# Kernel optimization log

Measured on AMD Instinct MI355X. Metric: run time of the kernel, lower is better.

The kernel has to match this reference:

```python
import jax, jax.numpy as jnp
import numpy as np

D = 16        # d_model
DFF = 128     # ffn hidden
H_NN = 128    # pairwise-MLP hidden
RES = 1.0     # res_ratio (undefined global in source; standard residual)
EPS = 1e-6


def setup_inputs() -> dict:
    key = jax.random.key(0)
    ks = jax.random.split(key, 16)
    B, G, L = 8, 1, 256
    def n(k, shape, s=0.05):
        return jax.random.normal(k, shape, jnp.float32) * s
    return dict(
        x=jax.random.normal(ks[0], (B, G, L, D), jnp.float32),
        mask=jnp.zeros((B, G, L, L), jnp.float32),
        wq=n(ks[1], (D, D)), bq=jnp.zeros((D,), jnp.float32),
        wk=n(ks[2], (D, D)), bk=jnp.zeros((D,), jnp.float32),
        wv=n(ks[3], (D, D)), bv=jnp.zeros((D,), jnp.float32),
        wo=n(ks[4], (D, D)), bo=jnp.zeros((D,), jnp.float32),
        nn_w1=n(ks[5], (2 * D, H_NN)), nn_b1=jnp.zeros((H_NN,), jnp.float32),
        nn_w2=n(ks[6], (H_NN, 1)), nn_b2=jnp.zeros((1,), jnp.float32),
        f1=n(ks[7], (D, DFF)), f1b=jnp.zeros((DFF,), jnp.float32),
        f2=n(ks[8], (DFF, D)), f2b=jnp.zeros((D,), jnp.float32),
        g1=jnp.ones((D,), jnp.float32), be1=jnp.zeros((D,), jnp.float32),
        g2=jnp.ones((D,), jnp.float32), be2=jnp.zeros((D,), jnp.float32),
    )


def _layernorm(x, g, b):
    m = jnp.mean(x, -1, keepdims=True)
    v = jnp.var(x, -1, keepdims=True)
    return (x - m) * jax.lax.rsqrt(v + EPS) * g + b


def reference(x, mask, wq, bq, wk, bk, wv, bv, wo, bo,
              nn_w1, nn_b1, nn_w2, nn_b2,
              f1, f1b, f2, f2b, g1, be1, g2, be2):
    # projections: (B,G,L,D)
    q = x @ wq + bq
    k = x @ wk + bk
    v = x @ wv + bv
    # pairwise relation-network attention.
    # NN(concat([q_i, k_j])) first layer splits as q_i @ W1[:D] + k_j @ W1[D:]
    w1q, w1k = nn_w1[:D], nn_w1[D:]
    w2 = nn_w2[:, 0]
    qa = q @ w1q  # (B,G,L,H)
    kb = k @ w1k
    h1 = jax.nn.relu(qa[:, :, :, None, :] + kb[:, :, None, :, :] + nn_b1)  # (B,G,Lq,Lk,H)
    logits = jnp.einsum('bgijh,h->bgij', h1, w2) + nn_b2[0]
    # make_sym: NN(concat([k_j, q_i])) -> k_j @ W1[:D] + q_i @ W1[D:]
    ka = k @ w1q
    qb = q @ w1k
    h2 = jax.nn.relu(qb[:, :, :, None, :] + ka[:, :, None, :, :] + nn_b1)
    logits = logits + jnp.einsum('bgijh,h->bgij', h2, w2) + nn_b2[0]
    logits = logits + mask * -1e9
    attn = jax.nn.softmax(logits, axis=-1)          # (B,G,Lq,Lk)
    ctx = jnp.einsum('bgij,bgjd->bgid', attn, v)    # (B,G,L,D)
    attn_out = ctx @ wo + bo
    out1 = _layernorm(RES * x + (2.0 - RES) * attn_out, g1, be1)
    ffn = jax.nn.relu(out1 @ f1 + f1b) @ f2 + f2b
    out2 = _layernorm(RES * out1 + (2.0 - RES) * ffn, g2, be2)
    return out2
```

## Files before the change

kernel.cpp:

```cpp
#include <hip/hip_runtime.h>
#include <hip/hip_bf16.h>

typedef __hip_bfloat16 bf16;
typedef float f32x4 __attribute__((ext_vector_type(4)));

constexpr int DIM  = 16;
constexpr int HNN  = 128;
constexpr int SEQ  = 256;
constexpr int BAT  = 8;
constexpr int ROWS = BAT * SEQ;
constexpr int HP   = HNN / 2;
constexpr int QT   = 4;
constexpr int NQT  = ROWS / QT;

__device__ __forceinline__ bool is_f32(const void* g1) {
  return ((const unsigned*)g1)[0] == 0x3F800000u;
}
__device__ __forceinline__ float ld(const void* p, long i, bool f32) {
  return f32 ? ((const float*)p)[i]
             : __bfloat162float(((const bf16*)p)[i]);
}

__global__ __launch_bounds__(128) void prep_kernel(
    const void* __restrict__ x,
    const void* __restrict__ wq, const void* __restrict__ bq,
    const void* __restrict__ wk, const void* __restrict__ bk,
    const void* __restrict__ wv, const void* __restrict__ bv,
    const void* __restrict__ nn_w1, const void* __restrict__ nn_b1,
    const void* __restrict__ nn_w2, const void* __restrict__ g1flag,
    float* __restrict__ kkT, float* __restrict__ qq,
    float* __restrict__ vT,  float2* __restrict__ w2p)
{
  const bool f32 = is_f32(g1flag);
  const int row = blockIdx.x;
  const int tid = threadIdx.x;
  __shared__ float xs[DIM], qs[DIM], ks[DIM], vs[DIM];

  if (tid < DIM) xs[tid] = ld(x, (long)row * DIM + tid, f32);
  __syncthreads();

  if (tid < 3 * DIM) {
    const int which = tid >> 4, d = tid & 15;
    const void* w  = (which == 0) ? wq : (which == 1) ? wk : wv;
    const void* bb = (which == 0) ? bq : (which == 1) ? bk : bv;
    float acc = ld(bb, d, f32);
    #pragma unroll
    for (int e = 0; e < DIM; e++) acc += xs[e] * ld(w, e * DIM + d, f32);
    if (which == 0) qs[d] = acc;
    else if (which == 1) ks[d] = acc;
    else vs[d] = acc;
  }
  __syncthreads();

  float qw1q = 0.f, qw1k = 0.f, kw1q = 0.f, kw1k = 0.f;
  #pragma unroll
  for (int d = 0; d < DIM; d++) {
    float a = ld(nn_w1, d * HNN + tid, f32);
    float b = ld(nn_w1, (DIM + d) * HNN + tid, f32);
    qw1q += qs[d] * a;  qw1k += qs[d] * b;
    kw1q += ks[d] * a;  kw1k += ks[d] * b;
  }
  const float b1 = ld(nn_b1, tid, f32);
  const int hp = tid >> 1, half = tid & 1;
  ((float2*)kkT)[((size_t)hp * ROWS + row) * 2 + half] =
      make_float2(kw1k + b1, kw1q + b1);
  ((float2*)qq)[((size_t)row * HP + hp) * 2 + half] =
      make_float2(qw1q, qw1k);
  if (tid < DIM) vT[tid * ROWS + row] = vs[tid];
  if (row == 0 && tid < HP)
    w2p[tid] = make_float2(ld(nn_w2, 2 * tid, f32), ld(nn_w2, 2 * tid + 1, f32));
}

__global__ __launch_bounds__(256) void fused_kernel(
    const void* __restrict__ x,  const void* __restrict__ mask,
    const void* __restrict__ wo, const void* __restrict__ bo,
    const void* __restrict__ nn_b2,
    const void* __restrict__ f1, const void* __restrict__ f1b,
    const void* __restrict__ f2, const void* __restrict__ f2b,
    const void* __restrict__ g1, const void* __restrict__ be1,
    const void* __restrict__ g2, const void* __restrict__ be2,
    const f32x4* __restrict__ kkT, const f32x4* __restrict__ qq,
    const float2* __restrict__ w2p, const float* __restrict__ vT,
    void* __restrict__ out)
{
  const bool f32 = is_f32(g1);
  const int qt   = blockIdx.x;
  const int bi   = qt >> 6;
  const int i0   = (qt & 63) * QT;
  const int row0 = bi * SEQ + i0;
  const int j    = threadIdx.x;
  const int col  = bi * SEQ + j;
  const int lane = j & 63, wv = j >> 6;

  __shared__ float pb[QT][SEQ];
  __shared__ float vbuf[SEQ][DIM + 1];
  __shared__ float cpart[QT][DIM][17];
  __shared__ float mxs[QT], sums[QT];
  __shared__ float ctxs[QT][DIM], o1s[QT][DIM], rrs[QT][DIM];
  __shared__ float hid[QT][HNN];

  #pragma unroll
  for (int d = 0; d < DIM; ++d) vbuf[j][d] = vT[d * ROWS + col];

  const f32x4* kkbase = kkT + col;
  const f32x4* q0b = qq + (size_t)(row0 + 0) * HP;
  const f32x4* q1b = qq + (size_t)(row0 + 1) * HP;
  const f32x4* q2b = qq + (size_t)(row0 + 2) * HP;
  const f32x4* q3b = qq + (size_t)(row0 + 3) * HP;

  const f32x4 z = {0.f, 0.f, 0.f, 0.f};
  f32x4 a0 = z, a1 = z, a2 = z, a3 = z;

  #pragma unroll 4
  for (int m = 0; m < HP; ++m) {
    const f32x4 kk = kkbase[(size_t)m * ROWS];
    const float2 w = w2p[m];
    const f32x4 w4 = {w.x, w.x, w.y, w.y};
    const f32x4 q0 = q0b[m];
    const f32x4 q1 = q1b[m];
    const f32x4 q2 = q2b[m];
    const f32x4 q3 = q3b[m];
    a0 = __builtin_elementwise_fma(__builtin_elementwise_max(q0 + kk, z), w4, a0);
    a1 = __builtin_elementwise_fma(__builtin_elementwise_max(q1 + kk, z), w4, a1);
    a2 = __builtin_elementwise_fma(__builtin_elementwise_max(q2 + kk, z), w4, a2);
    a3 = __builtin_elementwise_fma(__builtin_elementwise_max(q3 + kk, z), w4, a3);
  }

  const float b2 = 2.f * ld(nn_b2, 0, f32);
  float l0 = a0.x + a0.y + a0.z + a0.w + b2
           + ld(mask, (size_t)(row0 + 0) * SEQ + j, f32) * -1e9f;
  float l1 = a1.x + a1.y + a1.z + a1.w + b2
           + ld(mask, (size_t)(row0 + 1) * SEQ + j, f32) * -1e9f;
  float l2 = a2.x + a2.y + a2.z + a2.w + b2
           + ld(mask, (size_t)(row0 + 2) * SEQ + j, f32) * -1e9f;
  float l3 = a3.x + a3.y + a3.z + a3.w + b2
           + ld(mask, (size_t)(row0 + 3) * SEQ + j, f32) * -1e9f;

  pb[0][j] = l0; pb[1][j] = l1; pb[2][j] = l2; pb[3][j] = l3;
  __syncthreads();

  {
    float m4 = fmaxf(fmaxf(pb[wv][lane],       pb[wv][lane + 64]),
                     fmaxf(pb[wv][lane + 128], pb[wv][lane + 192]));
    #pragma unroll
    for (int off = 32; off > 0; off >>= 1) m4 = fmaxf(m4, __shfl_xor(m4, off, 64));
    if (lane == 0) mxs[wv] = m4;
  }
  __syncthreads();
  pb[0][j] = __expf(l0 - mxs[0]);
  pb[1][j] = __expf(l1 - mxs[1]);
  pb[2][j] = __expf(l2 - mxs[2]);
  pb[3][j] = __expf(l3 - mxs[3]);
  __syncthreads();
  {
    float s4 = pb[wv][lane] + pb[wv][lane + 64]
             + pb[wv][lane + 128] + pb[wv][lane + 192];
    #pragma unroll
    for (int off = 32; off > 0; off >>= 1) s4 += __shfl_xor(s4, off, 64);
    if (lane == 0) sums[wv] = s4;
  }
  __syncthreads();

  {
    const int d = j & 15, c = j >> 4;
    #pragma unroll
    for (int i = 0; i < QT; ++i) {
      float s = 0.f;
      #pragma unroll
      for (int jj = 0; jj < 16; ++jj)
        s += pb[i][c * 16 + jj] * vbuf[c * 16 + jj][d];
      cpart[i][d][c] = s;
    }
  }
  __syncthreads();
  if (j < QT * DIM) {
    const int i = j >> 4, d = j & 15;
    float s = 0.f;
    #pragma unroll
    for (int c = 0; c < 16; ++c) s += cpart[i][d][c];
    ctxs[i][d] = s / sums[i];
  }
  __syncthreads();

  if (j < QT * DIM) {
    const int i = j >> 4, d = j & 15;
    float ao = ld(bo, d, f32);
    #pragma unroll
    for (int dd = 0; dd < DIM; ++dd) ao += ctxs[i][dd] * ld(wo, dd * DIM + d, f32);
    rrs[i][d] = ld(x, (long)(row0 + i) * DIM + d, f32) + ao;
  }
  __syncthreads();
  if (j < QT * DIM) {
    const int i = j >> 4, d = j & 15;
    float mn = 0.f;
    #pragma unroll
    for (int dd = 0; dd < DIM; ++dd) mn += rrs[i][dd];
    mn *= (1.f / DIM);
    float vv = 0.f;
    #pragma unroll
    for (int dd = 0; dd < DIM; ++dd) { float zz = rrs[i][dd] - mn; vv += zz * zz; }
    vv *= (1.f / DIM);
    o1s[i][d] = (rrs[i][d] - mn) * rsqrtf(vv + 1e-6f) * ld(g1, d, f32)
              + ld(be1, d, f32);
  }
  __syncthreads();

  #pragma unroll
  for (int r = 0; r < 2; ++r) {
    const int u = r * 256 + j;
    const int i = u >> 7, h = u & 127;
    float a = ld(f1b, h, f32);
    #pragma unroll
    for (int dd = 0; dd < DIM; ++dd) a += o1s[i][dd] * ld(f1, dd * HNN + h, f32);
    hid[i][h] = fmaxf(a, 0.f);
  }
  __syncthreads();

  {
    const int d = j & 15, c = j >> 4;
    #pragma unroll
    for (int i = 0; i < QT; ++i) {
      float a = 0.f;
      #pragma unroll
      for (int hh = 0; hh < 8; ++hh) {
        const int h = c * 8 + hh;
        a += hid[i][h] * ld(f2, h * DIM + d, f32);
      }
      cpart[i][d][c] = a;
    }
  }
  __syncthreads();
  if (j < QT * DIM) {
    const int i = j >> 4, d = j & 15;
    float a = ld(f2b, d, f32);
    #pragma unroll
    for (int c = 0; c < 16; ++c) a += cpart[i][d][c];
    rrs[i][d] = o1s[i][d] + a;
  }
  __syncthreads();

  if (j < QT * DIM) {
    const int i = j >> 4, d = j & 15;
    float mn = 0.f;
    #pragma unroll
    for (int dd = 0; dd < DIM; ++dd) mn += rrs[i][dd];
    mn *= (1.f / DIM);
    float vv = 0.f;
    #pragma unroll
    for (int dd = 0; dd < DIM; ++dd) { float zz = rrs[i][dd] - mn; vv += zz * zz; }
    vv *= (1.f / DIM);
    const float val = (rrs[i][d] - mn) * rsqrtf(vv + 1e-6f) * ld(g2, d, f32)
                    + ld(be2, d, f32);
    const long oidx = (long)(row0 + i) * DIM + d;
    if (f32) ((float*)out)[oidx] = val;
    else     ((bf16*)out)[oidx] = __float2bfloat16(val);
  }
}

extern "C" void kernel_launch(void* const* d_in, const int* in_sizes, int n_in,
                              void* d_out, int out_size, void* d_ws, size_t ws_size,
                              hipStream_t stream) {
  const void* x     = d_in[0];
  const void* mask  = d_in[1];
  const void* wq    = d_in[2];
  const void* bq    = d_in[3];
  const void* wk    = d_in[4];
  const void* bk    = d_in[5];
  const void* wv    = d_in[6];
  const void* bv    = d_in[7];
  const void* wo    = d_in[8];
  const void* bo    = d_in[9];
  const void* nn_w1 = d_in[10];
  const void* nn_b1 = d_in[11];
  const void* nn_w2 = d_in[12];
  const void* nn_b2 = d_in[13];
  const void* f1    = d_in[14];
  const void* f1b   = d_in[15];
  const void* f2    = d_in[16];
  const void* f2b   = d_in[17];
  const void* g1    = d_in[18];
  const void* be1   = d_in[19];
  const void* g2    = d_in[20];
  const void* be2   = d_in[21];

  float*  kkT = (float*)d_ws;
  float*  qq  = kkT + (size_t)HP * ROWS * 4;
  float*  vT  = qq  + (size_t)ROWS * HP * 4;
  float2* w2p = (float2*)(vT + (size_t)DIM * ROWS);

  prep_kernel<<<ROWS, 128, 0, stream>>>(x, wq, bq, wk, bk, wv, bv,
                                        nn_w1, nn_b1, nn_w2, g1,
                                        kkT, qq, vT, w2p);
  fused_kernel<<<NQT, 256, 0, stream>>>(x, mask, wo, bo, nn_b2,
                                        f1, f1b, f2, f2b, g1, be1, g2, be2,
                                        (const f32x4*)kkT, (const f32x4*)qq,
                                        (const float2*)w2p, vT, d_out);
}
```

Baseline: 122.3 us.

## Assign one wavefront per query row and replace block barriers with shuffles

After the logits barrier, each of the four wavefronts now handles one query row on its own: softmax, the context reduction, the output projection, both layernorms and the FFN, all using wave shuffles and a per-row shared buffer. This drops about ten __syncthreads and the shared partial-sum arrays, and the partially idle block phases where only 64 threads worked. Block indexing is also interleaved across batches (bi = b&7) to change how blocks map to batch rows. The trade-off is more serial work per lane in the context and FFN loops, plus reliance on wave-level LDS visibility without a barrier.

Result: faster. 118.3 us (-3.2%).

```diff
diff --git a/kernel.cpp b/kernel.cpp
--- a/kernel.cpp
+++ b/kernel.cpp
@@ -84,9 +84,9 @@
     void* __restrict__ out)
 {
   const bool f32 = is_f32(g1);
-  const int qt   = blockIdx.x;
-  const int bi   = qt >> 6;
-  const int i0   = (qt & 63) * QT;
+  const int b    = blockIdx.x;
+  const int bi   = b & 7;
+  const int i0   = (b >> 3) * QT;
   const int row0 = bi * SEQ + i0;
   const int j    = threadIdx.x;
   const int col  = bi * SEQ + j;
@@ -94,10 +94,7 @@
 
   __shared__ float pb[QT][SEQ];
   __shared__ float vbuf[SEQ][DIM + 1];
-  __shared__ float cpart[QT][DIM][17];
-  __shared__ float mxs[QT], sums[QT];
-  __shared__ float ctxs[QT][DIM], o1s[QT][DIM], rrs[QT][DIM];
-  __shared__ float hid[QT][HNN];
+  __shared__ float hidw[QT][HNN];
 
   #pragma unroll
   for (int d = 0; d < DIM; ++d) vbuf[j][d] = vT[d * ROWS + col];
@@ -127,131 +124,95 @@
   }
 
   const float b2 = 2.f * ld(nn_b2, 0, f32);
-  float l0 = a0.x + a0.y + a0.z + a0.w + b2
-           + ld(mask, (size_t)(row0 + 0) * SEQ + j, f32) * -1e9f;
-  float l1 = a1.x + a1.y + a1.z + a1.w + b2
-           + ld(mask, (size_t)(row0 + 1) * SEQ + j, f32) * -1e9f;
-  float l2 = a2.x + a2.y + a2.z + a2.w + b2
-           + ld(mask, (size_t)(row0 + 2) * SEQ + j, f32) * -1e9f;
-  float l3 = a3.x + a3.y + a3.z + a3.w + b2
-           + ld(mask, (size_t)(row0 + 3) * SEQ + j, f32) * -1e9f;
+  const float l0 = a0.x + a0.y + a0.z + a0.w + b2
+                 + ld(mask, (size_t)(row0 + 0) * SEQ + j, f32) * -1e9f;
+  const float l1 = a1.x + a1.y + a1.z + a1.w + b2
+                 + ld(mask, (size_t)(row0 + 1) * SEQ + j, f32) * -1e9f;
+  const float l2 = a2.x + a2.y + a2.z + a2.w + b2
+                 + ld(mask, (size_t)(row0 + 2) * SEQ + j, f32) * -1e9f;
+  const float l3 = a3.x + a3.y + a3.z + a3.w + b2
+                 + ld(mask, (size_t)(row0 + 3) * SEQ + j, f32) * -1e9f;
 
   pb[0][j] = l0; pb[1][j] = l1; pb[2][j] = l2; pb[3][j] = l3;
   __syncthreads();
 
-  {
-    float m4 = fmaxf(fmaxf(pb[wv][lane],       pb[wv][lane + 64]),
-                     fmaxf(pb[wv][lane + 128], pb[wv][lane + 192]));
-    #pragma unroll
-    for (int off = 32; off > 0; off >>= 1) m4 = fmaxf(m4, __shfl_xor(m4, off, 64));
-    if (lane == 0) mxs[wv] = m4;
-  }
-  __syncthreads();
-  pb[0][j] = __expf(l0 - mxs[0]);
-  pb[1][j] = __expf(l1 - mxs[1]);
-  pb[2][j] = __expf(l2 - mxs[2]);
-  pb[3][j] = __expf(l3 - mxs[3]);
-  __syncthreads();
-  {
-    float s4 = pb[wv][lane] + pb[wv][lane + 64]
-             + pb[wv][lane + 128] + pb[wv][lane + 192];
-    #pragma unroll
-    for (int off = 32; off > 0; off >>= 1) s4 += __shfl_xor(s4, off, 64);
-    if (lane == 0) sums[wv] = s4;
-  }
-  __syncthreads();
-
-  {
-    const int d = j & 15, c = j >> 4;
-    #pragma unroll
-    for (int i = 0; i < QT; ++i) {
-      float s = 0.f;
-      #pragma unroll
-      for (int jj = 0; jj < 16; ++jj)
-        s += pb[i][c * 16 + jj] * vbuf[c * 16 + jj][d];
-      cpart[i][d][c] = s;
-    }
-  }
-  __syncthreads();
-  if (j < QT * DIM) {
-    const int i = j >> 4, d = j & 15;
-    float s = 0.f;
-    #pragma unroll
-    for (int c = 0; c < 16; ++c) s += cpart[i][d][c];
-    ctxs[i][d] = s / sums[i];
-  }
-  __syncthreads();
-
-  if (j < QT * DIM) {
-    const int i = j >> 4, d = j & 15;
-    float ao = ld(bo, d, f32);
-    #pragma unroll
-    for (int dd = 0; dd < DIM; ++dd) ao += ctxs[i][dd] * ld(wo, dd * DIM + d, f32);
-    rrs[i][d] = ld(x, (long)(row0 + i) * DIM + d, f32) + ao;
-  }
-  __syncthreads();
-  if (j < QT * DIM) {
-    const int i = j >> 4, d = j & 15;
-    float mn = 0.f;
-    #pragma unroll
-    for (int dd = 0; dd < DIM; ++dd) mn += rrs[i][dd];
-    mn *= (1.f / DIM);
-    float vv = 0.f;
-    #pragma unroll
-    for (int dd = 0; dd < DIM; ++dd) { float zz = rrs[i][dd] - mn; vv += zz * zz; }
-    vv *= (1.f / DIM);
-    o1s[i][d] = (rrs[i][d] - mn) * rsqrtf(vv + 1e-6f) * ld(g1, d, f32)
-              + ld(be1, d, f32);
-  }
-  __syncthreads();
-
-  #pragma unroll
-  for (int r = 0; r < 2; ++r) {
-    const int u = r * 256 + j;
-    const int i = u >> 7, h = u & 127;
-    float a = ld(f1b, h, f32);
-    #pragma unroll
-    for (int dd = 0; dd < DIM; ++dd) a += o1s[i][dd] * ld(f1, dd * HNN + h, f32);
-    hid[i][h] = fmaxf(a, 0.f);
-  }
-  __syncthreads();
-
-  {
-    const int d = j & 15, c = j >> 4;
-    #pragma unroll
-    for (int i = 0; i < QT; ++i) {
-      float a = 0.f;
-      #pragma unroll
-      for (int hh = 0; hh < 8; ++hh) {
-        const int h = c * 8 + hh;
-        a += hid[i][h] * ld(f2, h * DIM + d, f32);
-      }
-      cpart[i][d][c] = a;
-    }
-  }
-  __syncthreads();
-  if (j < QT * DIM) {
-    const int i = j >> 4, d = j & 15;
-    float a = ld(f2b, d, f32);
-    #pragma unroll
-    for (int c = 0; c < 16; ++c) a += cpart[i][d][c];
-    rrs[i][d] = o1s[i][d] + a;
-  }
-  __syncthreads();
-
-  if (j < QT * DIM) {
-    const int i = j >> 4, d = j & 15;
-    float mn = 0.f;
-    #pragma unroll
-    for (int dd = 0; dd < DIM; ++dd) mn += rrs[i][dd];
-    mn *= (1.f / DIM);
-    float vv = 0.f;
-    #pragma unroll
-    for (int dd = 0; dd < DIM; ++dd) { float zz = rrs[i][dd] - mn; vv += zz * zz; }
-    vv *= (1.f / DIM);
-    const float val = (rrs[i][d] - mn) * rsqrtf(vv + 1e-6f) * ld(g2, d, f32)
-                    + ld(be2, d, f32);
-    const long oidx = (long)(row0 + i) * DIM + d;
+  const int  i    = wv;
+  const long grow = row0 + i;
+
+  float lc0 = pb[i][lane],       lc1 = pb[i][lane + 64];
+  float lc2 = pb[i][lane + 128], lc3 = pb[i][lane + 192];
+  float mx = fmaxf(fmaxf(lc0, lc1), fmaxf(lc2, lc3));
+  #pragma unroll
+  for (int off = 32; off > 0; off >>= 1) mx = fmaxf(mx, __shfl_xor(mx, off, 64));
+  const float e0 = __expf(lc0 - mx), e1 = __expf(lc1 - mx);
+  const float e2 = __expf(lc2 - mx), e3 = __expf(lc3 - mx);
+  float s = e0 + e1 + e2 + e3;
+  #pragma unroll
+  for (int off = 32; off > 0; off >>= 1) s += __shfl_xor(s, off, 64);
+  const float inv = 1.f / s;
+  pb[i][lane] = e0; pb[i][lane + 64] = e1;
+  pb[i][lane + 128] = e2; pb[i][lane + 192] = e3;
+
+  const int d = lane & 15, cq = lane >> 4;
+  float cs = 0.f;
+  #pragma unroll
+  for (int jj = 0; jj < 64; ++jj) {
+    const int jx = cq * 64 + ((jj + cq * 16) & 63);
+    cs += pb[i][jx] * vbuf[jx][d];
+  }
+  cs += __shfl_xor(cs, 16, 64);
+  cs += __shfl_xor(cs, 32, 64);
+  const float ctxv = cs * inv;
+
+  float ao = ld(bo, d, f32);
+  #pragma unroll
+  for (int dd = 0; dd < DIM; ++dd)
+    ao += __shfl(ctxv, dd, 64) * ld(wo, dd * DIM + d, f32);
+  const float rr = ld(x, grow * DIM + d, f32) + ao;
+
+  float mn = rr;
+  mn += __shfl_xor(mn, 1, 64); mn += __shfl_xor(mn, 2, 64);
+  mn += __shfl_xor(mn, 4, 64); mn += __shfl_xor(mn, 8, 64);
+  mn *= (1.f / DIM);
+  float z1 = rr - mn;
+  float vv = z1 * z1;
+  vv += __shfl_xor(vv, 1, 64); vv += __shfl_xor(vv, 2, 64);
+  vv += __shfl_xor(vv, 4, 64); vv += __shfl_xor(vv, 8, 64);
+  vv *= (1.f / DIM);
+  const float o1v = z1 * rsqrtf(vv + 1e-6f) * ld(g1, d, f32) + ld(be1, d, f32);
+
+  float h0 = ld(f1b, lane, f32), h1 = ld(f1b, lane + 64, f32);
+  #pragma unroll
+  for (int dd = 0; dd < DIM; ++dd) {
+    const float ov = __shfl(o1v, dd, 64);
+    h0 += ov * ld(f1, dd * HNN + lane, f32);
+    h1 += ov * ld(f1, dd * HNN + lane + 64, f32);
+  }
+  hidw[i][lane]      = fmaxf(h0, 0.f);
+  hidw[i][lane + 64] = fmaxf(h1, 0.f);
+
+  float fa = 0.f;
+  #pragma unroll
+  for (int hh = 0; hh < 32; ++hh) {
+    const int h = cq * 32 + ((hh + cq * 8) & 31);
+    fa += hidw[i][h] * ld(f2, h * DIM + d, f32);
+  }
+  fa += __shfl_xor(fa, 16, 64);
+  fa += __shfl_xor(fa, 32, 64);
+  const float r2 = o1v + ld(f2b, d, f32) + fa;
+
+  float mn2 = r2;
+  mn2 += __shfl_xor(mn2, 1, 64); mn2 += __shfl_xor(mn2, 2, 64);
+  mn2 += __shfl_xor(mn2, 4, 64); mn2 += __shfl_xor(mn2, 8, 64);
+  mn2 *= (1.f / DIM);
+  float z2 = r2 - mn2;
+  float v2 = z2 * z2;
+  v2 += __shfl_xor(v2, 1, 64); v2 += __shfl_xor(v2, 2, 64);
+  v2 += __shfl_xor(v2, 4, 64); v2 += __shfl_xor(v2, 8, 64);
+  v2 *= (1.f / DIM);
+  const float val = z2 * rsqrtf(v2 + 1e-6f) * ld(g2, d, f32) + ld(be2, d, f32);
+  if (cq == 0) {
+    const long oidx = grow * DIM + d;
     if (f32) ((float*)out)[oidx] = val;
     else     ((bf16*)out)[oidx] = __float2bfloat16(val);
   }
```
